# Optimization experiments

Measured on AMD Instinct MI355X. Metric: run time of the kernel, lower is better.

Reference implementation:

```python
import jax, jax.numpy as jnp
import numpy as np

IN_FEATURES = 4096
OUT_FEATURES = 11008
N_TOKENS = 8192


def setup_inputs() -> dict:
    key = jax.random.key(0)
    kx, kw, kb = jax.random.split(key, 3)
    x = jax.random.normal(kx, (N_TOKENS, IN_FEATURES), dtype=jnp.float32)
    # nn.Linear weight: [out_features, in_features]
    bound = 1.0 / np.sqrt(IN_FEATURES)
    weight = jax.random.uniform(kw, (OUT_FEATURES, IN_FEATURES), dtype=jnp.float32,
                                minval=-bound, maxval=bound)
    bias = jax.random.uniform(kb, (OUT_FEATURES,), dtype=jnp.float32,
                              minval=-bound, maxval=bound)
    return {"x": x, "weight": weight, "bias": bias}


def reference(x, weight, bias):
    # Ternarize weights to {-1, 0, +1} then standard dense matmul + bias.
    ternary_w = jnp.sign(weight)  # [out, in]
    return jnp.matmul(x, ternary_w.T) + bias  # [n_tokens, out]
```

## Files before the change

### kernel.cpp

```cpp
#include <hip/hip_runtime.h>
#include <stdint.h>

#define M_DIM 8192
#define N_DIM 11008
#define K_DIM 4096

#define BM 256
#define BN 256
#define BK 64
#define NT (K_DIM / BK)
#define GRID_M (M_DIM / BM)
#define GRID_N (N_DIM / BN)
#define NWG (GRID_M * GRID_N)

#define BUF (BM * BK)
#define NRING 5

typedef int i32x4 __attribute__((ext_vector_type(4)));

__device__ __forceinline__ void gload16(const int8_t* src, int8_t* dst) {
    __builtin_amdgcn_global_load_lds(
        (const __attribute__((address_space(1))) uint32_t*)src,
        (__attribute__((address_space(3))) uint32_t*)dst, 16, 0, 0);
}


__global__ __launch_bounds__(256) void quant_x_kernel(
    const float* __restrict__ x, int8_t* __restrict__ xq, float* __restrict__ sinv)
{
    const int wave = blockIdx.x * 4 + (threadIdx.x >> 6);
    const int lane = threadIdx.x & 63;
    const float* row = x + (size_t)wave * K_DIM;

    float4 v[16];
    float mx = 0.0f;
    #pragma unroll
    for (int j = 0; j < 16; ++j) {
        v[j] = *(const float4*)(row + (j * 64 + lane) * 4);
        mx = fmaxf(mx, fmaxf(fmaxf(fabsf(v[j].x), fabsf(v[j].y)),
                             fmaxf(fabsf(v[j].z), fabsf(v[j].w))));
    }
    #pragma unroll
    for (int off = 32; off > 0; off >>= 1)
        mx = fmaxf(mx, __shfl_xor(mx, off));
    if (mx < 1e-30f) mx = 1e-30f;
    const float s = 127.0f / mx;

    int8_t* orow = xq + (size_t)wave * K_DIM;
    #pragma unroll
    for (int j = 0; j < 16; ++j) {
        int a = (int)__builtin_rintf(v[j].x * s);
        int b = (int)__builtin_rintf(v[j].y * s);
        int c = (int)__builtin_rintf(v[j].z * s);
        int d = (int)__builtin_rintf(v[j].w * s);
        uint32_t p = (uint32_t)(a & 0xFF) | ((uint32_t)(b & 0xFF) << 8) |
                     ((uint32_t)(c & 0xFF) << 16) | ((uint32_t)(d & 0xFF) << 24);
        *(uint32_t*)(orow + (j * 64 + lane) * 4) = p;
    }
    if (lane == 0) sinv[wave] = mx / 127.0f;
}


__global__ __launch_bounds__(256) void sign_w_kernel(
    const float* __restrict__ w, int8_t* __restrict__ wq, long long n16)
{
    long long i = (long long)blockIdx.x * blockDim.x + threadIdx.x;
    const long long stride = (long long)gridDim.x * blockDim.x;
    for (; i < n16; i += stride) {
        const float* src = w + i * 16;
        uint32_t pk[4];
        #pragma unroll
        for (int q = 0; q < 4; ++q) {
            float4 f = *(const float4*)(src + q * 4);
            int a = (f.x > 0.f) ? 1 : ((f.x < 0.f) ? -1 : 0);
            int b = (f.y > 0.f) ? 1 : ((f.y < 0.f) ? -1 : 0);
            int c = (f.z > 0.f) ? 1 : ((f.z < 0.f) ? -1 : 0);
            int d = (f.w > 0.f) ? 1 : ((f.w < 0.f) ? -1 : 0);
            pk[q] = (uint32_t)(a & 0xFF) | ((uint32_t)(b & 0xFF) << 8) |
                    ((uint32_t)(c & 0xFF) << 16) | ((uint32_t)(d & 0xFF) << 24);
        }
        *(i32x4*)(wq + i * 16) = (i32x4){(int)pk[0], (int)pk[1], (int)pk[2], (int)pk[3]};
    }
}


__global__ __launch_bounds__(512, 2) void ternary_gemm_i8(
    const int8_t* __restrict__ A, const int8_t* __restrict__ B,
    const float* __restrict__ bias, const float* __restrict__ sinv,
    float* __restrict__ out)
{
    extern __shared__ int8_t lds[];
    int8_t* As = lds;
    int8_t* Bs = lds + NRING * BUF;

    const int tid  = threadIdx.x;
    const int lane = tid & 63;
    const int wid  = tid >> 6;
    const int wm   = wid >> 2;
    const int wn   = wid & 3;
    const int l15  = lane & 15;
    const int l4   = lane >> 4;

    const int bid = blockIdx.x;
    const int swz = (bid & 7) * (NWG / 8) + (bid >> 3);
    const int bm  = swz / GRID_N;
    const int bn  = swz % GRID_N;
    const long brow = (long)bm * BM;
    const long bcol = (long)bn * BN;

    const int rowt = tid >> 2;
    const int ssrc = (tid & 3) ^ ((tid >> 3) & 3);
    const int8_t* pA = A + (size_t)(brow + rowt) * K_DIM + ssrc * 16;
    const int8_t* pB = B + (size_t)(bcol + rowt) * K_DIM + ssrc * 16;

    auto stageAB = [&](int t, int bslot) {
        #pragma unroll
        for (int r = 0; r < 2; ++r)
            gload16(pA + (size_t)r * 128 * K_DIM + (size_t)t * BK,
                    As + bslot * BUF + r * 8192 + wid * 1024 + (lane << 4));
        #pragma unroll
        for (int r = 0; r < 2; ++r)
            gload16(pB + (size_t)r * 128 * K_DIM + (size_t)t * BK,
                    Bs + bslot * BUF + r * 8192 + wid * 1024 + (lane << 4));
    };

    const int slot = l4 ^ ((l15 >> 1) & 3);
    const int aOff = (wm * 16 + l15) * 64 + slot * 16;
    const int bOff = (wn * 16 + l15) * 64 + slot * 16;

    i32x4 acc[8][4];
    #pragma unroll
    for (int m = 0; m < 8; ++m)
        #pragma unroll
        for (int n = 0; n < 4; ++n) acc[m][n] = (i32x4){0, 0, 0, 0};

    i32x4 arA[8], brA[4], arB[8], brB[4];

    auto readFragsS = [&](int s, i32x4 (&ar)[8], i32x4 (&br)[4]) {
        const int8_t* Ab = As + s * BUF;
        const int8_t* Bb = Bs + s * BUF;
        #pragma unroll
        for (int m = 0; m < 8; ++m) ar[m] = *(const i32x4*)(Ab + m * 2048 + aOff);
        #pragma unroll
        for (int n = 0; n < 4; ++n) br[n] = *(const i32x4*)(Bb + n * 4096 + bOff);
    };

    stageAB(0, 0); stageAB(1, 1); stageAB(2, 2); stageAB(3, 3);
    asm volatile("s_waitcnt vmcnt(8)" ::: "memory");
    __builtin_amdgcn_s_barrier();
    __builtin_amdgcn_sched_barrier(0);
    readFragsS(0, arA, brA);

    int sn = 1;
    int ss = 4;

    auto body = [&](int t, i32x4 (&arc)[8], i32x4 (&brc)[4],
                           i32x4 (&arn)[8], i32x4 (&brn)[4]) {
        if (t + 1 < NT) readFragsS(sn, arn, brn);
        if (t + 4 < NT) stageAB(t + 4, ss);

        __builtin_amdgcn_s_setprio(1);
        #pragma unroll
        for (int m = 0; m < 8; ++m)
            #pragma unroll
            for (int n = 0; n < 4; ++n)
                acc[m][n] = __builtin_amdgcn_mfma_i32_16x16x64_i8(arc[m], brc[n], acc[m][n], 0, 0, 0);
        __builtin_amdgcn_s_setprio(0);

        asm volatile("s_waitcnt lgkmcnt(12)" ::: "memory");
        __builtin_amdgcn_sched_barrier(0);
        if (t <= NT - 5)      { asm volatile("s_waitcnt vmcnt(8)" ::: "memory"); }
        else if (t == NT - 4) { asm volatile("s_waitcnt vmcnt(4)" ::: "memory"); }
        else                  { asm volatile("s_waitcnt vmcnt(0)" ::: "memory"); }
        __builtin_amdgcn_s_barrier();
        __builtin_amdgcn_sched_barrier(0);

        sn = (sn == NRING - 1) ? 0 : sn + 1;
        ss = (ss == NRING - 1) ? 0 : ss + 1;
    };

    for (int t = 0; t < NT; t += 2) {
        body(t,     arA, brA, arB, brB);
        body(t + 1, arB, brB, arA, brA);
    }

    int   cols[4];
    float bv[4];
    #pragma unroll
    for (int n = 0; n < 4; ++n) {
        cols[n] = (int)bcol + n * 64 + wn * 16 + l15;
        bv[n] = bias[cols[n]];
    }
    #pragma unroll
    for (int m = 0; m < 8; ++m) {
        const size_t row0 = (size_t)brow + m * 32 + wm * 16 + l4 * 4;
        float s0 = sinv[row0], s1 = sinv[row0 + 1], s2 = sinv[row0 + 2], s3 = sinv[row0 + 3];
        #pragma unroll
        for (int n = 0; n < 4; ++n) {
            out[(row0 + 0) * N_DIM + cols[n]] = (float)acc[m][n][0] * s0 + bv[n];
            out[(row0 + 1) * N_DIM + cols[n]] = (float)acc[m][n][1] * s1 + bv[n];
            out[(row0 + 2) * N_DIM + cols[n]] = (float)acc[m][n][2] * s2 + bv[n];
            out[(row0 + 3) * N_DIM + cols[n]] = (float)acc[m][n][3] * s3 + bv[n];
        }
    }
}


__global__ void naive_kernel(const float* __restrict__ x, const float* __restrict__ w,
                             const float* __restrict__ bias, float* __restrict__ out) {
    long long o = (long long)blockIdx.x * blockDim.x + threadIdx.x;
    if (o >= (long long)M_DIM * N_DIM) return;
    int row = (int)(o / N_DIM), col = (int)(o % N_DIM);
    float s = 0.0f;
    const float* xr = x + (size_t)row * K_DIM;
    const float* wr = w + (size_t)col * K_DIM;
    for (int k = 0; k < K_DIM; ++k) {
        float wv = wr[k];
        s += (wv > 0.0f) ? xr[k] : ((wv < 0.0f) ? -xr[k] : 0.0f);
    }
    out[o] = s + bias[col];
}


extern "C" void kernel_launch(void* const* d_in, const int* in_sizes, int n_in,
                              void* d_out, int out_size, void* d_ws, size_t ws_size,
                              hipStream_t stream) {
    const float* x    = (const float*)d_in[0];
    const float* w    = (const float*)d_in[1];
    const float* bias = (const float*)d_in[2];
    float* out        = (float*)d_out;

    const size_t xq_bytes = (size_t)M_DIM * K_DIM;
    const size_t wq_bytes = (size_t)N_DIM * K_DIM;
    const size_t si_bytes = (size_t)M_DIM * sizeof(float);

    if (ws_size >= xq_bytes + wq_bytes + si_bytes) {
        int8_t* xq   = (int8_t*)d_ws;
        int8_t* wq   = (int8_t*)((char*)d_ws + xq_bytes);
        float*  sinv = (float*)((char*)d_ws + xq_bytes + wq_bytes);

        quant_x_kernel<<<M_DIM / 4, 256, 0, stream>>>(x, xq, sinv);
        const long long n16 = ((long long)N_DIM * K_DIM) / 16;
        sign_w_kernel<<<2048, 256, 0, stream>>>(w, wq, n16);

        const int lds_bytes = NRING * 2 * BUF;
        hipFuncSetAttribute(reinterpret_cast<const void*>(ternary_gemm_i8),
                            hipFuncAttributeMaxDynamicSharedMemorySize, lds_bytes);
        ternary_gemm_i8<<<NWG, 512, lds_bytes, stream>>>(xq, wq, bias, sinv, out);
    } else {
        const long long total = (long long)M_DIM * N_DIM;
        naive_kernel<<<(int)((total + 255) / 256), 256, 0, stream>>>(x, w, bias, out);
    }
}
```

Baseline: 479.4 us.

## Stagger LDS fragment reads between wave groups to spread LDS traffic

Splits waves by wm into two schedules. One group issues the next LDS fragment reads before its MFMAs; the other runs half its MFMAs first, then the reads, then the rest. The aim is to offset LDS read bursts across waves so they contend less and overlap better with MFMA work. It also reorders reads so B fragments load first, and it drops the explicit lgkmcnt(12) wait. Removing that wait leaves the LDS-read ordering to the compiler's implicit waits, which is a possible correctness or stall risk.

New measurement: 481.2 us. No clear change (+0.4%).

```diff
diff --git a/kernel.cpp b/kernel.cpp
--- a/kernel.cpp
+++ b/kernel.cpp
@@ -140,9 +140,19 @@
         const int8_t* Ab = As + s * BUF;
         const int8_t* Bb = Bs + s * BUF;
         #pragma unroll
+        for (int n = 0; n < 4; ++n) br[n] = *(const i32x4*)(Bb + n * 4096 + bOff);
+        #pragma unroll
         for (int m = 0; m < 8; ++m) ar[m] = *(const i32x4*)(Ab + m * 2048 + aOff);
-        #pragma unroll
-        for (int n = 0; n < 4; ++n) br[n] = *(const i32x4*)(Bb + n * 4096 + bOff);
+    };
+
+    auto mfmaHalf = [&](i32x4 (&arc)[8], i32x4 (&brc)[4], int m0, int m1) {
+        __builtin_amdgcn_s_setprio(1);
+        #pragma unroll
+        for (int m = m0; m < m1; ++m)
+            #pragma unroll
+            for (int n = 0; n < 4; ++n)
+                acc[m][n] = __builtin_amdgcn_mfma_i32_16x16x64_i8(arc[m], brc[n], acc[m][n], 0, 0, 0);
+        __builtin_amdgcn_s_setprio(0);
     };
 
     stageAB(0, 0); stageAB(1, 1); stageAB(2, 2); stageAB(3, 3);
@@ -150,38 +160,51 @@
     __builtin_amdgcn_s_barrier();
     __builtin_amdgcn_sched_barrier(0);
     readFragsS(0, arA, brA);
+    __builtin_amdgcn_sched_barrier(0);
 
     int sn = 1;
     int ss = 4;
 
-    auto body = [&](int t, i32x4 (&arc)[8], i32x4 (&brc)[4],
-                           i32x4 (&arn)[8], i32x4 (&brn)[4]) {
-        if (t + 1 < NT) readFragsS(sn, arn, brn);
+    auto boundary = [&](int t) {
         if (t + 4 < NT) stageAB(t + 4, ss);
-
-        __builtin_amdgcn_s_setprio(1);
-        #pragma unroll
-        for (int m = 0; m < 8; ++m)
-            #pragma unroll
-            for (int n = 0; n < 4; ++n)
-                acc[m][n] = __builtin_amdgcn_mfma_i32_16x16x64_i8(arc[m], brc[n], acc[m][n], 0, 0, 0);
-        __builtin_amdgcn_s_setprio(0);
-
-        asm volatile("s_waitcnt lgkmcnt(12)" ::: "memory");
         __builtin_amdgcn_sched_barrier(0);
         if (t <= NT - 5)      { asm volatile("s_waitcnt vmcnt(8)" ::: "memory"); }
         else if (t == NT - 4) { asm volatile("s_waitcnt vmcnt(4)" ::: "memory"); }
         else                  { asm volatile("s_waitcnt vmcnt(0)" ::: "memory"); }
         __builtin_amdgcn_s_barrier();
         __builtin_amdgcn_sched_barrier(0);
-
         sn = (sn == NRING - 1) ? 0 : sn + 1;
         ss = (ss == NRING - 1) ? 0 : ss + 1;
     };
 
-    for (int t = 0; t < NT; t += 2) {
-        body(t,     arA, brA, arB, brB);
-        body(t + 1, arB, brB, arA, brA);
+    if (wm == 0) {
+        auto bodyE = [&](int t, i32x4 (&arc)[8], i32x4 (&brc)[4],
+                                i32x4 (&arn)[8], i32x4 (&brn)[4]) {
+            if (t + 1 < NT) readFragsS(sn, arn, brn);
+            __builtin_amdgcn_sched_barrier(0);
+            mfmaHalf(arc, brc, 0, 8);
+            __builtin_amdgcn_sched_barrier(0);
+            boundary(t);
+        };
+        for (int t = 0; t < NT; t += 2) {
+            bodyE(t,     arA, brA, arB, brB);
+            bodyE(t + 1, arB, brB, arA, brA);
+        }
+    } else {
+        auto bodyO = [&](int t, i32x4 (&arc)[8], i32x4 (&brc)[4],
+                                i32x4 (&arn)[8], i32x4 (&brn)[4]) {
+            mfmaHalf(arc, brc, 0, 4);
+            __builtin_amdgcn_sched_barrier(0);
+            if (t + 1 < NT) readFragsS(sn, arn, brn);
+            __builtin_amdgcn_sched_barrier(0);
+            mfmaHalf(arc, brc, 4, 8);
+            __builtin_amdgcn_sched_barrier(0);
+            boundary(t);
+        };
+        for (int t = 0; t < NT; t += 2) {
+            bodyO(t,     arA, brA, arB, brB);
+            bodyO(t + 1, arB, brB, arA, brA);
+        }
     }
 
     int   cols[4];
```
